# Kernel optimization log

Hardware: AMD Instinct MI355X
Metric: run time of the kernel (lower is better)

## Reference

```python
import jax, jax.numpy as jnp
import numpy as np

EMBED_DIM = 1024
NUM_HEADS = 16
HEAD_DIM = EMBED_DIM // NUM_HEADS
BATCH = 4
SEQ = 2048


def setup_inputs() -> dict:
    key = jax.random.key(0)
    k1, k2, k3 = jax.random.split(key, 3)
    scale = 0.02
    x = jax.random.normal(k1, (BATCH, SEQ, EMBED_DIM), dtype=jnp.float32)
    Wqkv = jax.random.normal(k2, (EMBED_DIM, 3 * EMBED_DIM), dtype=jnp.float32) * scale
    bqkv = jnp.zeros((3 * EMBED_DIM,), dtype=jnp.float32)
    Wout = jax.random.normal(k3, (EMBED_DIM, EMBED_DIM), dtype=jnp.float32) * scale
    bout = jnp.zeros((EMBED_DIM,), dtype=jnp.float32)
    # causal mask: 1 where attention is allowed (lower triangle), 0 elsewhere
    mask = jnp.tril(jnp.ones((SEQ, SEQ), dtype=jnp.int32))
    return {"x": x, "mask": mask, "Wqkv": Wqkv, "bqkv": bqkv, "Wout": Wout, "bout": bout}


def reference(x, mask, Wqkv, bqkv, Wout, bout):
    B, S, E = x.shape
    H, D = NUM_HEADS, HEAD_DIM
    qkv = x @ Wqkv + bqkv                      # [B,S,3E]
    qkv = qkv.reshape(B, S, 3, H, D)
    qkv = jnp.transpose(qkv, (2, 0, 3, 1, 4))  # [3,B,H,S,D]
    Q, K, V = qkv[0], qkv[1], qkv[2]
    scores = jnp.einsum('bhqd,bhkd->bhqk', Q, K) / jnp.sqrt(jnp.float32(D))
    scores = jnp.where(mask[None, None] == 0, jnp.float32(-jnp.inf), scores)
    attn = jax.nn.softmax(scores, axis=-1)     # dropout omitted (eval mode)
    out = jnp.einsum('bhqk,bhkd->bhqd', attn, V)
    out = jnp.transpose(out, (0, 2, 1, 3)).reshape(B, S, E)
    return out @ Wout + bout
```

## Files before the change

### kernel.cpp

```cpp
#include <hip/hip_runtime.h>

#define S_LEN 2048
#define NH    16
#define HD    64
#define EMB   1024
#define NB    4
#define MROWS (NB * S_LEN)

typedef __attribute__((ext_vector_type(8))) short  short8;
typedef __attribute__((ext_vector_type(4))) float  float4_t;
typedef __attribute__((ext_vector_type(4))) int    int4_t;
union U8 { int4_t i; short8 s; };

__device__ __forceinline__ unsigned short f2bf(float f) {
    unsigned int x = __float_as_uint(f);
    unsigned int r = (x + 0x7fffu + ((x >> 16) & 1u)) >> 16;
    return (unsigned short)r;
}

__device__ __forceinline__ unsigned int cvtpk_bf16(float lo, float hi) {
    unsigned int r;
    asm("v_cvt_pk_bf16_f32 %0, %1, %2" : "=v"(r) : "v"(lo), "v"(hi));
    return r;
}

typedef const __attribute__((address_space(1))) unsigned int* gas_ptr;
typedef __attribute__((address_space(3))) unsigned int*       las_ptr;
__device__ __forceinline__ void gld_lds16(const void* g, void* l) {
    __builtin_amdgcn_global_load_lds((gas_ptr)g, (las_ptr)l, 16, 0, 0);
}

template<bool B> struct BoolC { static constexpr bool v = B; };

#define QSCALE 0.18033688011112042f

__global__ __launch_bounds__(256) void prep(
    const float* __restrict__ x,    unsigned short* __restrict__ Xb,
    const float* __restrict__ Wqkv, unsigned short* __restrict__ WqkvT,
    const float* __restrict__ Wout, unsigned short* __restrict__ WoutT)
{
    __shared__ float tile[32][33];
    int bid = blockIdx.x, t = threadIdx.x;
    if (bid < 16384) {
        int i = bid * 256 + t;
        float2 v = ((const float2*)x)[i];
        ushort2 o; o.x = f2bf(v.x); o.y = f2bf(v.y);
        ((ushort2*)Xb)[i] = o;
        return;
    }
    const float* in; unsigned short* out; int R, C, n0, r0;
    if (bid < 19456) {
        int b2 = bid - 16384;
        in = Wqkv; out = WqkvT; R = EMB; C = 3 * EMB;
        n0 = (b2 % 96) * 32; r0 = (b2 / 96) * 32;
    } else {
        int b2 = bid - 19456;
        in = Wout; out = WoutT; R = EMB; C = EMB;
        n0 = (b2 & 31) * 32; r0 = (b2 >> 5) * 32;
    }
    int tx = t & 31, ty = t >> 5;
#pragma unroll
    for (int i = 0; i < 4; ++i)
        tile[ty + i * 8][tx] = in[(size_t)(r0 + ty + i * 8) * C + n0 + tx];
    __syncthreads();
#pragma unroll
    for (int i = 0; i < 4; ++i)
        out[(size_t)(n0 + ty + i * 8) * R + r0 + tx] = f2bf(tile[tx][ty + i * 8]);
}

__global__ __launch_bounds__(256, 2) void gemm_qkv(
    const unsigned short* __restrict__ X,
    const unsigned short* __restrict__ WT,
    const float* __restrict__ bias,
    unsigned short* __restrict__ Qb,
    unsigned short* __restrict__ Kb,
    unsigned short* __restrict__ VTb)
{
    __shared__ alignas(16) unsigned short smem[24576];
    const int K = 1024;
    const int NT = K / 32;
    int t = threadIdx.x;
    int wave = t >> 6, lane = t & 63, quad = lane >> 4, l = lane & 15;
    int bm = blockIdx.x * 128, bn = blockIdx.y * 128;
    int wm = (wave >> 1) * 64, wn = (wave & 1) * 64;
    int colrd = (quad ^ ((l >> 1) & 3)) * 8;

    float4_t z = {0.f, 0.f, 0.f, 0.f};
    float4_t acc[4][4];
#pragma unroll
    for (int i = 0; i < 4; ++i)
#pragma unroll
        for (int j = 0; j < 4; ++j) acc[i][j] = z;

    auto stage = [&](int kt, int slot) {
        int k0 = kt * 32;
        unsigned short* Ad = smem + slot * 4096;
        unsigned short* Bd = smem + 12288 + slot * 4096;
#pragma unroll
        for (int it = 0; it < 2; ++it) {
            int c = t + 256 * it;
            int row = c >> 2;
            int col = ((c & 3) ^ ((c >> 3) & 3)) * 8;
            gld_lds16(&X [(size_t)(bm + row) * K + k0 + col], &Ad[c * 8]);
            gld_lds16(&WT[(size_t)(bn + row) * K + k0 + col], &Bd[c * 8]);
        }
    };

    auto compute = [&](int slot) {
        const unsigned short* Ac = smem + slot * 4096;
        const unsigned short* Bc = smem + 12288 + slot * 4096;
        short8 af[4], bfr[4];
#pragma unroll
        for (int i = 0; i < 4; ++i)
            af[i] = *(const short8*)&Ac[(wm + i * 16 + l) * 32 + colrd];
#pragma unroll
        for (int j = 0; j < 4; ++j)
            bfr[j] = *(const short8*)&Bc[(wn + j * 16 + l) * 32 + colrd];
#pragma unroll
        for (int i = 0; i < 4; ++i)
#pragma unroll
            for (int j = 0; j < 4; ++j)
                acc[i][j] = __builtin_amdgcn_mfma_f32_16x16x32_bf16(
                    af[i], bfr[j], acc[i][j], 0, 0, 0);
    };

    stage(0, 0);
    stage(1, 1);
    int cs = 0, ss = 2;
    for (int u = 0; u < NT; ++u) {
        if (u + 1 < NT) {
            asm volatile("s_waitcnt vmcnt(4)" ::: "memory");
        } else {
            asm volatile("s_waitcnt vmcnt(0)" ::: "memory");
        }
        __builtin_amdgcn_s_barrier();
        __builtin_amdgcn_sched_barrier(0);
        if (u + 2 < NT) stage(u + 2, ss);
        compute(cs);
        cs = (cs == 2) ? 0 : cs + 1;
        ss = (ss == 2) ? 0 : ss + 1;
    }

    __syncthreads();
    int which = bn >> 10;
    int bnr = bn & 1023;
    int b = bm >> 11;
    if (which == 2) {
#pragma unroll
        for (int j = 0; j < 4; ++j) {
            float bv = bias[bn + wn + j * 16 + l];
            int c = wn + j * 16 + l;
#pragma unroll
            for (int i = 0; i < 4; ++i) {
                uint2 vv;
                vv.x = cvtpk_bf16(acc[i][j][0] + bv, acc[i][j][1] + bv);
                vv.y = cvtpk_bf16(acc[i][j][2] + bv, acc[i][j][3] + bv);
                *(uint2*)&smem[c * 132 + wm + quad * 16 + i * 4] = vv;
            }
        }
        __syncthreads();
        int sbase = bm & 2047;
#pragma unroll
        for (int pass = 0; pass < 8; ++pass) {
            int c = pass * 16 + (t >> 4);
            int sp = (t & 15) * 8;
            int rem = bnr + c, h = rem >> 6, d = rem & 63;
            uint2 lo = *(const uint2*)&smem[c * 132 + sp];
            uint2 hi = *(const uint2*)&smem[c * 132 + sp + 4];
            int4_t v = {(int)lo.x, (int)lo.y, (int)hi.x, (int)hi.y};
            *(int4_t*)&VTb[((size_t)(b * NH + h) * HD + d) * S_LEN + sbase + sp] = v;
        }
    } else {
#pragma unroll
        for (int j = 0; j < 4; ++j) {
            float bv = bias[bn + wn + j * 16 + l];
            int c = wn + j * 16 + l;
#pragma unroll
            for (int i = 0; i < 4; ++i)
#pragma unroll
                for (int r = 0; r < 4; ++r) {
                    float ov = acc[i][j][r] + bv;
                    if (which == 0) ov *= QSCALE;
                    smem[(wm + i * 16 + quad * 4 + r) * 132 + c] = f2bf(ov);
                }
        }
        __syncthreads();
        unsigned short* dst = which ? Kb : Qb;
        int s0g = bm & 2047;
#pragma unroll
        for (int pass = 0; pass < 8; ++pass) {
            int s = pass * 16 + (t >> 4);
            int cp = (t & 15) * 8;
            int rem = bnr + cp, h = rem >> 6, d = rem & 63;
            uint2 lo = *(const uint2*)&smem[s * 132 + cp];
            uint2 hi = *(const uint2*)&smem[s * 132 + cp + 4];
            int4_t v = {(int)lo.x, (int)lo.y, (int)hi.x, (int)hi.y};
            *(int4_t*)&dst[((size_t)(b * NH + h) * S_LEN + s0g + s) * HD + d] = v;
        }
    }
}

__global__ __launch_bounds__(256, 2) void flash_attn(
    const unsigned short* __restrict__ Qb,
    const unsigned short* __restrict__ Kb,
    const unsigned short* __restrict__ VTb,
    unsigned short* __restrict__ AO)
{
    __shared__ alignas(16) unsigned short smem[24576];

    int t = threadIdx.x, wave = t >> 6, lane = t & 63, quad = lane >> 4, cl = lane & 15;
    int blk = blockIdx.x;
    int bh = (blk & 7) + 8 * ((blk >> 3) & 7);
    int g = blk >> 6;
    int b = bh >> 4, h = bh & 15;
    int ci = (wave & 2) ? (62 - 2 * g + (wave & 1)) : (2 * g + (wave & 1));
    int qb = 32 * ci;
    int nkt = (ci >> 1) + 1;
    int nkt_max = 32 - g;

    const unsigned short* Qbase = Qb  + (size_t)bh * S_LEN * HD;
    const unsigned short* Kbase = Kb  + (size_t)bh * S_LEN * HD;
    const unsigned short* Vbase = VTb + (size_t)bh * HD * S_LEN;

    float4_t z = {0.f, 0.f, 0.f, 0.f};
    short8 onesf;
#pragma unroll
    for (int i = 0; i < 8; ++i) onesf[i] = (short)0x3F80;

    short8 bQ[2][2];
#pragma unroll
    for (int qt = 0; qt < 2; ++qt)
#pragma unroll
        for (int hh = 0; hh < 2; ++hh)
            bQ[qt][hh] = *(const short8*)&Qbase[(size_t)(qb + qt * 16 + cl) * HD + hh * 32 + quad * 8];

    float4_t acc[2][4], accs[2];
#pragma unroll
    for (int qt = 0; qt < 2; ++qt) {
        accs[qt] = z;
#pragma unroll
        for (int nb = 0; nb < 4; ++nb) acc[qt][nb] = z;
    }

    int koff0[4], koff1[4];
#pragma unroll
    for (int t4 = 0; t4 < 4; ++t4) {
        int row = t4 * 16 + cl, sw = row & 7;
        koff0[t4] = (row << 7) | ((quad ^ sw) << 4);
        koff1[t4] = (row << 7) | (((quad + 4) ^ sw) << 4);
    }
    int voffB[2][4];
#pragma unroll
    for (int p = 0; p < 2; ++p)
#pragma unroll
        for (int nb = 0; nb < 4; ++nb) {
            int row = nb * 16 + cl;
            voffB[p][nb] = 8192 + ((row << 7) | (((quad * 2 + p) ^ (row & 7)) << 4));
        }

    auto stage = [&](int kt, int slot) {
        int key0 = kt << 6;
        unsigned short* Kd = smem + slot * 8192;
        unsigned short* Vd = Kd + 4096;
#pragma unroll
        for (int i = 0; i < 2; ++i) {
            int s = t + 256 * i;
            int row = s >> 3, c16 = (s & 7) ^ (row & 7);
            gld_lds16(&Kbase[(size_t)(key0 + row) * HD + c16 * 8], &Kd[s * 8]);
            gld_lds16(&Vbase[(size_t)row * S_LEN + key0 + c16 * 8], &Vd[s * 8]);
        }
    };

    auto compute = [&](auto DIAGC, int slot, int key0) {
        constexpr bool DIAG = decltype(DIAGC)::v;
        const char* Kc = (const char*)(smem + slot * 8192);
        short8 aK0[4], aK1[4];
#pragma unroll
        for (int t4 = 0; t4 < 4; ++t4) {
            aK0[t4] = *(const short8*)(Kc + koff0[t4]);
            aK1[t4] = *(const short8*)(Kc + koff1[t4]);
        }
        U8 bv[2][4];
#pragma unroll
        for (int p = 0; p < 2; ++p)
#pragma unroll
            for (int nb = 0; nb < 4; ++nb)
                bv[p][nb].i = *(const int4_t*)(Kc + voffB[p][nb]);

#pragma unroll
        for (int qt = 0; qt < 2; ++qt) {
            unsigned int pk[4][2];
#pragma unroll
            for (int t4 = 0; t4 < 4; ++t4) {
                float4_t st = __builtin_amdgcn_mfma_f32_16x16x32_bf16(
                    aK1[t4], bQ[qt][1],
                    __builtin_amdgcn_mfma_f32_16x16x32_bf16(aK0[t4], bQ[qt][0], z, 0, 0, 0),
                    0, 0, 0);
                float e[4];
#pragma unroll
                for (int r = 0; r < 4; ++r) {
                    e[r] = __builtin_amdgcn_exp2f(st[r]);
                    if (DIAG) {
                        int key = key0 + t4 * 16 + quad * 4 + r;
                        e[r] = (key <= qb + qt * 16 + cl) ? e[r] : 0.f;
                    }
                }
                pk[t4][0] = cvtpk_bf16(e[0], e[1]);
                pk[t4][1] = cvtpk_bf16(e[2], e[3]);
            }
#pragma unroll
            for (int p = 0; p < 2; ++p) {
                U8 a; a.i = (int4_t){(int)pk[2 * p][0], (int)pk[2 * p][1],
                                     (int)pk[2 * p + 1][0], (int)pk[2 * p + 1][1]};
                accs[qt] = __builtin_amdgcn_mfma_f32_16x16x32_bf16(
                    a.s, onesf, accs[qt], 0, 0, 0);
#pragma unroll
                for (int nb = 0; nb < 4; ++nb)
                    acc[qt][nb] = __builtin_amdgcn_mfma_f32_16x16x32_bf16(
                        a.s, bv[p][nb].s, acc[qt][nb], 0, 0, 0);
            }
        }
    };

    stage(0, 0);
    if (nkt_max > 1) stage(1, 1);
    int cb = 0, sb = 2;
    for (int u = 0; u < nkt_max; ++u) {
        if (u + 1 < nkt_max) {
            asm volatile("s_waitcnt vmcnt(4)" ::: "memory");
        } else {
            asm volatile("s_waitcnt vmcnt(0)" ::: "memory");
        }
        __builtin_amdgcn_s_barrier();
        __builtin_amdgcn_sched_barrier(0);
        if (u + 2 < nkt_max) stage(u + 2, sb);
        if (u < nkt) {
            if (u == nkt - 1) compute(BoolC<true>{},  cb, u << 6);
            else              compute(BoolC<false>{}, cb, u << 6);
        }
        cb = (cb == 2) ? 0 : cb + 1;
        sb = (sb == 2) ? 0 : sb + 1;
    }

    __syncthreads();
    unsigned short* stgw = smem + wave * 1088;

#pragma unroll
    for (int qt = 0; qt < 2; ++qt) {
        float fr[4];
#pragma unroll
        for (int r = 0; r < 4; ++r) fr[r] = 1.f / accs[qt][r];
#pragma unroll
        for (int nb = 0; nb < 4; ++nb)
#pragma unroll
            for (int r = 0; r < 4; ++r) {
                unsigned int uu = __float_as_uint(acc[qt][nb][r] * fr[r]) + 0x8000u;
                stgw[(quad * 4 + r) * 68 + nb * 16 + cl] = (unsigned short)(uu >> 16);
            }
#pragma unroll
        for (int pass = 0; pass < 4; ++pass) {
            int idx = pass * 64 + lane;
            int row = idx >> 4, part = idx & 15;
            ushort4 v = *(const ushort4*)&stgw[row * 68 + part * 4];
            *(ushort4*)&AO[((size_t)b * S_LEN + qb + qt * 16 + row) * EMB + h * HD + part * 4] = v;
        }
    }
}

__global__ __launch_bounds__(256, 2) void gemm_out(
    const unsigned short* __restrict__ A,
    const unsigned short* __restrict__ WT,
    const float* __restrict__ bias,
    float* __restrict__ out)
{
    __shared__ alignas(16) unsigned short smemA[3 * 4096];
    __shared__ alignas(16) unsigned short smemB[3 * 4096];
    const int K = 1024;
    const int NT = K / 32;
    int t = threadIdx.x;
    int wave = t >> 6, lane = t & 63, quad = lane >> 4, l = lane & 15;
    int bm = blockIdx.x * 128, bn = blockIdx.y * 128;
    int wm = (wave >> 1) * 64, wn = (wave & 1) * 64;
    int colrd = (quad ^ ((l >> 1) & 3)) * 8;

    float4_t z = {0.f, 0.f, 0.f, 0.f};
    float4_t acc[4][4];
#pragma unroll
    for (int i = 0; i < 4; ++i)
#pragma unroll
        for (int j = 0; j < 4; ++j) acc[i][j] = z;

    auto stage = [&](int kt, int slot) {
        int k0 = kt * 32;
        unsigned short* Ad = smemA + slot * 4096;
        unsigned short* Bd = smemB + slot * 4096;
#pragma unroll
        for (int it = 0; it < 2; ++it) {
            int c = t + 256 * it;
            int row = c >> 2;
            int col = ((c & 3) ^ ((c >> 3) & 3)) * 8;
            gld_lds16(&A [(size_t)(bm + row) * K + k0 + col], &Ad[c * 8]);
            gld_lds16(&WT[(size_t)(bn + row) * K + k0 + col], &Bd[c * 8]);
        }
    };

    auto compute = [&](int slot) {
        const unsigned short* Ac = smemA + slot * 4096;
        const unsigned short* Bc = smemB + slot * 4096;
        short8 af[4], bfr[4];
#pragma unroll
        for (int i = 0; i < 4; ++i)
            af[i] = *(const short8*)&Ac[(wm + i * 16 + l) * 32 + colrd];
#pragma unroll
        for (int j = 0; j < 4; ++j)
            bfr[j] = *(const short8*)&Bc[(wn + j * 16 + l) * 32 + colrd];
#pragma unroll
        for (int i = 0; i < 4; ++i)
#pragma unroll
            for (int j = 0; j < 4; ++j)
                acc[i][j] = __builtin_amdgcn_mfma_f32_16x16x32_bf16(
                    af[i], bfr[j], acc[i][j], 0, 0, 0);
    };

    stage(0, 0);
    stage(1, 1);
    int cs = 0, ss = 2;
    for (int u = 0; u < NT; ++u) {
        if (u + 1 < NT) {
            asm volatile("s_waitcnt vmcnt(4)" ::: "memory");
        } else {
            asm volatile("s_waitcnt vmcnt(0)" ::: "memory");
        }
        __builtin_amdgcn_s_barrier();
        __builtin_amdgcn_sched_barrier(0);
        if (u + 2 < NT) stage(u + 2, ss);
        compute(cs);
        cs = (cs == 2) ? 0 : cs + 1;
        ss = (ss == 2) ? 0 : ss + 1;
    }

#pragma unroll
    for (int j = 0; j < 4; ++j) {
        int gc = bn + wn + j * 16 + l;
        float bv = bias[gc];
#pragma unroll
        for (int i = 0; i < 4; ++i) {
#pragma unroll
            for (int r = 0; r < 4; ++r) {
                int gr = bm + wm + i * 16 + quad * 4 + r;
                out[(size_t)gr * EMB + gc] = acc[i][j][r] + bv;
            }
        }
    }
}

extern "C" void kernel_launch(void* const* d_in, const int* in_sizes, int n_in,
                              void* d_out, int out_size, void* d_ws, size_t ws_size,
                              hipStream_t stream) {
    const float* x    = (const float*)d_in[0];
    const float* Wqkv = (const float*)d_in[2];
    const float* bqkv = (const float*)d_in[3];
    const float* Wout = (const float*)d_in[4];
    const float* bout = (const float*)d_in[5];
    float* out = (float*)d_out;

    char* ws = (char*)d_ws;
    const size_t SZ = (size_t)NB * NH * S_LEN * HD * 2;
    unsigned short* Qb    = (unsigned short*)(ws);
    unsigned short* Kb    = (unsigned short*)(ws + SZ);
    unsigned short* VTb   = (unsigned short*)(ws + 2 * SZ);
    unsigned short* Xb    = (unsigned short*)(ws + 3 * SZ);
    unsigned short* AO    = (unsigned short*)(ws + 3 * SZ);
    unsigned short* WqkvT = (unsigned short*)(ws + 4 * SZ);
    unsigned short* WoutT = (unsigned short*)(ws + 4 * SZ + (size_t)3 * EMB * EMB * 2);

    prep<<<dim3(20480), 256, 0, stream>>>(x, Xb, Wqkv, WqkvT, Wout, WoutT);
    gemm_qkv<<<dim3(MROWS / 128, 3 * EMB / 128), 256, 0, stream>>>(Xb, WqkvT, bqkv, Qb, Kb, VTb);
    flash_attn<<<dim3(1024), 256, 0, stream>>>(Qb, Kb, VTb, AO);
    gemm_out<<<dim3(MROWS / 128, EMB / 128), 256, 0, stream>>>(AO, WoutT, bout, out);
}
```

Measured before the change: 240.9 us.

## Use BK=64 double-buffered tiles with 8-way XOR swizzle in QKV and output GEMMs

Both projection GEMMs now stage 64-wide K slices instead of 32, with two LDS buffers in place of three and a new 8-column XOR swizzle for the wider rows. Halving the number of K iterations halves the barriers and waitcnt points per tile and gives each barrier interval twice the MFMA work. In exchange, prefetch depth drops from two stages to one and the loop waits on vmcnt(0) every step, so global-load latency is less hidden. LDS use per block grows to 64 KB.

Result: faster. 235.0 us (-2.5%).

```diff
diff --git a/kernel.cpp b/kernel.cpp
--- a/kernel.cpp
+++ b/kernel.cpp
@@ -76,14 +76,13 @@
     unsigned short* __restrict__ Kb,
     unsigned short* __restrict__ VTb)
 {
-    __shared__ alignas(16) unsigned short smem[24576];
+    __shared__ alignas(16) unsigned short smem[32768];
     const int K = 1024;
-    const int NT = K / 32;
+    const int NT = K / 64;
     int t = threadIdx.x;
     int wave = t >> 6, lane = t & 63, quad = lane >> 4, l = lane & 15;
     int bm = blockIdx.x * 128, bn = blockIdx.y * 128;
     int wm = (wave >> 1) * 64, wn = (wave & 1) * 64;
-    int colrd = (quad ^ ((l >> 1) & 3)) * 8;
 
     float4_t z = {0.f, 0.f, 0.f, 0.f};
     float4_t acc[4][4];
@@ -93,52 +92,48 @@
         for (int j = 0; j < 4; ++j) acc[i][j] = z;
 
     auto stage = [&](int kt, int slot) {
-        int k0 = kt * 32;
-        unsigned short* Ad = smem + slot * 4096;
-        unsigned short* Bd = smem + 12288 + slot * 4096;
-#pragma unroll
-        for (int it = 0; it < 2; ++it) {
+        int k0 = kt * 64;
+        unsigned short* Ad = smem + slot * 8192;
+        unsigned short* Bd = smem + 16384 + slot * 8192;
+#pragma unroll
+        for (int it = 0; it < 4; ++it) {
             int c = t + 256 * it;
-            int row = c >> 2;
-            int col = ((c & 3) ^ ((c >> 3) & 3)) * 8;
+            int row = c >> 3;
+            int col = ((c & 7) ^ (row & 7)) * 8;
             gld_lds16(&X [(size_t)(bm + row) * K + k0 + col], &Ad[c * 8]);
             gld_lds16(&WT[(size_t)(bn + row) * K + k0 + col], &Bd[c * 8]);
         }
     };
 
     auto compute = [&](int slot) {
-        const unsigned short* Ac = smem + slot * 4096;
-        const unsigned short* Bc = smem + 12288 + slot * 4096;
-        short8 af[4], bfr[4];
-#pragma unroll
-        for (int i = 0; i < 4; ++i)
-            af[i] = *(const short8*)&Ac[(wm + i * 16 + l) * 32 + colrd];
-#pragma unroll
-        for (int j = 0; j < 4; ++j)
-            bfr[j] = *(const short8*)&Bc[(wn + j * 16 + l) * 32 + colrd];
-#pragma unroll
-        for (int i = 0; i < 4; ++i)
+        const unsigned short* Ac = smem + slot * 8192;
+        const unsigned short* Bc = smem + 16384 + slot * 8192;
+#pragma unroll
+        for (int kk = 0; kk < 2; ++kk) {
+            int srd = ((kk * 4 + quad) ^ (l & 7)) * 8;
+            short8 af[4], bfr[4];
+#pragma unroll
+            for (int i = 0; i < 4; ++i)
+                af[i] = *(const short8*)&Ac[(wm + i * 16 + l) * 64 + srd];
 #pragma unroll
             for (int j = 0; j < 4; ++j)
-                acc[i][j] = __builtin_amdgcn_mfma_f32_16x16x32_bf16(
-                    af[i], bfr[j], acc[i][j], 0, 0, 0);
+                bfr[j] = *(const short8*)&Bc[(wn + j * 16 + l) * 64 + srd];
+#pragma unroll
+            for (int i = 0; i < 4; ++i)
+#pragma unroll
+                for (int j = 0; j < 4; ++j)
+                    acc[i][j] = __builtin_amdgcn_mfma_f32_16x16x32_bf16(
+                        af[i], bfr[j], acc[i][j], 0, 0, 0);
+        }
     };
 
     stage(0, 0);
-    stage(1, 1);
-    int cs = 0, ss = 2;
     for (int u = 0; u < NT; ++u) {
-        if (u + 1 < NT) {
-            asm volatile("s_waitcnt vmcnt(4)" ::: "memory");
-        } else {
-            asm volatile("s_waitcnt vmcnt(0)" ::: "memory");
-        }
+        asm volatile("s_waitcnt vmcnt(0)" ::: "memory");
         __builtin_amdgcn_s_barrier();
         __builtin_amdgcn_sched_barrier(0);
-        if (u + 2 < NT) stage(u + 2, ss);
-        compute(cs);
-        cs = (cs == 2) ? 0 : cs + 1;
-        ss = (ss == 2) ? 0 : ss + 1;
+        if (u + 1 < NT) stage(u + 1, (u + 1) & 1);
+        compute(u & 1);
     }
 
     __syncthreads();
@@ -373,15 +368,13 @@
     const float* __restrict__ bias,
     float* __restrict__ out)
 {
-    __shared__ alignas(16) unsigned short smemA[3 * 4096];
-    __shared__ alignas(16) unsigned short smemB[3 * 4096];
+    __shared__ alignas(16) unsigned short smem[32768];
     const int K = 1024;
-    const int NT = K / 32;
+    const int NT = K / 64;
     int t = threadIdx.x;
     int wave = t >> 6, lane = t & 63, quad = lane >> 4, l = lane & 15;
     int bm = blockIdx.x * 128, bn = blockIdx.y * 128;
     int wm = (wave >> 1) * 64, wn = (wave & 1) * 64;
-    int colrd = (quad ^ ((l >> 1) & 3)) * 8;
 
     float4_t z = {0.f, 0.f, 0.f, 0.f};
     float4_t acc[4][4];
@@ -391,52 +384,48 @@
         for (int j = 0; j < 4; ++j) acc[i][j] = z;
 
     auto stage = [&](int kt, int slot) {
-        int k0 = kt * 32;
-        unsigned short* Ad = smemA + slot * 4096;
-        unsigned short* Bd = smemB + slot * 4096;
-#pragma unroll
-        for (int it = 0; it < 2; ++it) {
+        int k0 = kt * 64;
+        unsigned short* Ad = smem + slot * 8192;
+        unsigned short* Bd = smem + 16384 + slot * 8192;
+#pragma unroll
+        for (int it = 0; it < 4; ++it) {
             int c = t + 256 * it;
-            int row = c >> 2;
-            int col = ((c & 3) ^ ((c >> 3) & 3)) * 8;
+            int row = c >> 3;
+            int col = ((c & 7) ^ (row & 7)) * 8;
             gld_lds16(&A [(size_t)(bm + row) * K + k0 + col], &Ad[c * 8]);
             gld_lds16(&WT[(size_t)(bn + row) * K + k0 + col], &Bd[c * 8]);
         }
     };
 
     auto compute = [&](int slot) {
-        const unsigned short* Ac = smemA + slot * 4096;
-        const unsigned short* Bc = smemB + slot * 4096;
-        short8 af[4], bfr[4];
-#pragma unroll
-        for (int i = 0; i < 4; ++i)
-            af[i] = *(const short8*)&Ac[(wm + i * 16 + l) * 32 + colrd];
-#pragma unroll
-        for (int j = 0; j < 4; ++j)
-            bfr[j] = *(const short8*)&Bc[(wn + j * 16 + l) * 32 + colrd];
-#pragma unroll
-        for (int i = 0; i < 4; ++i)
+        const unsigned short* Ac = smem + slot * 8192;
+        const unsigned short* Bc = smem + 16384 + slot * 8192;
+#pragma unroll
+        for (int kk = 0; kk < 2; ++kk) {
+            int srd = ((kk * 4 + quad) ^ (l & 7)) * 8;
+            short8 af[4], bfr[4];
+#pragma unroll
+            for (int i = 0; i < 4; ++i)
+                af[i] = *(const short8*)&Ac[(wm + i * 16 + l) * 64 + srd];
 #pragma unroll
             for (int j = 0; j < 4; ++j)
-                acc[i][j] = __builtin_amdgcn_mfma_f32_16x16x32_bf16(
-                    af[i], bfr[j], acc[i][j], 0, 0, 0);
+                bfr[j] = *(const short8*)&Bc[(wn + j * 16 + l) * 64 + srd];
+#pragma unroll
+            for (int i = 0; i < 4; ++i)
+#pragma unroll
+                for (int j = 0; j < 4; ++j)
+                    acc[i][j] = __builtin_amdgcn_mfma_f32_16x16x32_bf16(
+                        af[i], bfr[j], acc[i][j], 0, 0, 0);
+        }
     };
 
     stage(0, 0);
-    stage(1, 1);
-    int cs = 0, ss = 2;
     for (int u = 0; u < NT; ++u) {
-        if (u + 1 < NT) {
-            asm volatile("s_waitcnt vmcnt(4)" ::: "memory");
-        } else {
-            asm volatile("s_waitcnt vmcnt(0)" ::: "memory");
-        }
+        asm volatile("s_waitcnt vmcnt(0)" ::: "memory");
         __builtin_amdgcn_s_barrier();
         __builtin_amdgcn_sched_barrier(0);
-        if (u + 2 < NT) stage(u + 2, ss);
-        compute(cs);
-        cs = (cs == 2) ? 0 : cs + 1;
-        ss = (ss == 2) ? 0 : ss + 1;
+        if (u + 1 < NT) stage(u + 1, (u + 1) & 1);
+        compute(u & 1);
     }
 
 #pragma unroll
```
